# Performance work log

Hardware: AMD Instinct MI355X
Metric: run time of the kernel (lower is better)

Reference implementation:

```python
import jax, jax.numpy as jnp
import numpy as np

EPS = 1e-5

def _proj(x, w, b, gamma, beta, mean, var):
    # 1x1 conv (einsum over channels) + BatchNorm (inference) ; Dropout is identity in eval.
    y = jnp.einsum('bchw,oc->bohw', x, w) + b[None, :, None, None]
    scale = gamma * jax.lax.rsqrt(var + EPS)
    shift = beta - mean * scale
    return y * scale[None, :, None, None] + shift[None, :, None, None]

def _make_layer(key, cin, cout):
    k1, k2, k3, k4 = jax.random.split(key, 4)
    w = jax.random.normal(k1, (cout, cin), jnp.float32) * (1.0 / np.sqrt(cin))
    b = jax.random.normal(k2, (cout,), jnp.float32) * 0.01
    gamma = 1.0 + 0.1 * jax.random.normal(k3, (cout,), jnp.float32)
    beta = 0.1 * jax.random.normal(k4, (cout,), jnp.float32)
    mean = 0.05 * jax.random.normal(jax.random.fold_in(k1, 7), (cout,), jnp.float32)
    var = 0.5 + jax.random.uniform(jax.random.fold_in(k2, 7), (cout,), jnp.float32)
    return w, b, gamma, beta, mean, var

def setup_inputs() -> dict:
    key = jax.random.key(0)
    B, C, Ci, H, W = 4, 128, 64, 64, 64
    ks = jax.random.split(key, 6)
    inp = {
        'x1': jax.random.normal(ks[0], (B, C, H, W), jnp.float32),
        'x2': jax.random.normal(ks[1], (B, C, H, W), jnp.float32),
    }
    for name, k, cin, cout in [('theta', ks[2], C, Ci), ('phi', ks[3], C, Ci),
                               ('g', ks[4], C, Ci), ('wout', ks[5], Ci, C)]:
        w, b, gm, bt, mn, vr = _make_layer(k, cin, cout)
        inp.update({f'{name}_w': w, f'{name}_b': b, f'{name}_g': gm,
                    f'{name}_beta': bt, f'{name}_m': mn, f'{name}_v': vr})
    return inp

def reference(x1, x2,
              theta_w, theta_b, theta_g, theta_beta, theta_m, theta_v,
              phi_w, phi_b, phi_g, phi_beta, phi_m, phi_v,
              g_w, g_b, g_g, g_beta, g_m, g_v,
              wout_w, wout_b, wout_g, wout_beta, wout_m, wout_v):
    B, C, H, W = x1.shape
    N = H * W
    theta_x1 = _proj(x1, theta_w, theta_b, theta_g, theta_beta, theta_m, theta_v).reshape(B, -1, N)  # [B,Ci,N]
    phi_x2 = _proj(x2, phi_w, phi_b, phi_g, phi_beta, phi_m, phi_v).reshape(B, -1, N)                # [B,Ci,N]
    g_x2 = _proj(x2, g_w, g_b, g_g, g_beta, g_m, g_v).reshape(B, -1, N)                              # [B,Ci,N]
    # attention_map[b, n, m] = sum_c theta[b,c,n] * phi[b,c,m]
    attn = jax.nn.softmax(jnp.einsum('bcn,bcm->bnm', theta_x1, phi_x2), axis=-1)  # [B,N,N]
    out = jnp.einsum('bnm,bcm->bcn', attn, g_x2).reshape(B, -1, H, W)             # [B,Ci,H,W]
    out = _proj(out, wout_w, wout_b, wout_g, wout_beta, wout_m, wout_v)           # [B,C,H,W]
    return jnp.concatenate((out, x1), axis=1)                                     # [B,2C,H,W]
```

## Files before the change

### kernel.cpp

```cpp
#include <hip/hip_runtime.h>
#include <stdint.h>
#include <stddef.h>

#define EPS   1e-5f
#define CINCH 128
#define CI    64
#define NPIX  4096
#define KSPL  8
#define LOG2E 1.44269504088896340736f

typedef __bf16 bf16_t;
typedef _Float16 f16_t;
typedef bf16_t bf16x8 __attribute__((ext_vector_type(8)));
typedef f16_t  f16x8  __attribute__((ext_vector_type(8)));
typedef float  f32x4  __attribute__((ext_vector_type(4)));

typedef __attribute__((address_space(3))) unsigned int lds_u32;
typedef __attribute__((address_space(1))) const unsigned int glb_u32;

__device__ __forceinline__ f32x4 mfma16(bf16x8 a, bf16x8 b, f32x4 c) {
  return __builtin_amdgcn_mfma_f32_16x16x32_bf16(a, b, c, 0, 0, 0);
}
__device__ __forceinline__ f32x4 fzero4() {
  f32x4 z = {0.f, 0.f, 0.f, 0.f};
  return z;
}
__device__ __forceinline__ void gload16(const void* g, void* l) {
  __builtin_amdgcn_global_load_lds((glb_u32*)g, (lds_u32*)l, 16, 0, 0);
}


__global__ __launch_bounds__(256) void proj_theta(
    const float* __restrict__ x1,
    const float* __restrict__ w,  const float* __restrict__ bb,
    const float* __restrict__ gm, const float* __restrict__ bt,
    const float* __restrict__ mn, const float* __restrict__ vr,
    bf16_t* __restrict__ thetaT_h, bf16_t* __restrict__ thetaT_l,
    float* __restrict__ out)
{
  __shared__ float wT[CINCH][CI];
  __shared__ float bfold[CI];
  __shared__ __align__(16) char ubuf[CINCH * 32 * 4];
  float (*xs)[32]    = (float(*)[32])ubuf;
  float (*tileF)[68] = (float(*)[68])ubuf;

  const int tid = threadIdx.x;
  const int b   = blockIdx.y;
  const int n0  = blockIdx.x * 32;

  for (int idx = tid; idx < CI * CINCH; idx += 256) {
    const int o = idx & 63, c = idx >> 6;
    const float sc = gm[o] * rsqrtf(vr[o] + EPS);
    wT[c][o] = w[o * CINCH + c] * sc * LOG2E;
    if (c == 0) bfold[o] = (bb[o] * sc + bt[o] - mn[o] * sc) * LOG2E;
  }

  {
    const float* xsrc = x1 + (size_t)b * CINCH * NPIX + n0;
    float* osrc = out + ((size_t)b * 256 + 128) * NPIX + n0;
#pragma unroll
    for (int i = 0; i < 4; ++i) {
      const int idx = i * 256 + tid;
      const int c = idx >> 3, p = idx & 7;
      const f32x4 v = *(const f32x4*)(xsrc + (size_t)c * NPIX + p * 4);
      *(f32x4*)&xs[c][p * 4] = v;
      *(f32x4*)(osrc + (size_t)c * NPIX + p * 4) = v;
    }
  }
  __syncthreads();

  const int px = tid & 31;
  const int og = tid >> 5;
  float acc[8];
#pragma unroll
  for (int j = 0; j < 8; ++j) acc[j] = 0.f;

#pragma unroll 4
  for (int c0 = 0; c0 < CINCH; c0 += 4) {
    float xv[4];
#pragma unroll
    for (int cc = 0; cc < 4; ++cc) xv[cc] = xs[c0 + cc][px];
#pragma unroll
    for (int cc = 0; cc < 4; ++cc) {
      const f32x4 w0 = *(const f32x4*)&wT[c0 + cc][og * 8];
      const f32x4 w1 = *(const f32x4*)&wT[c0 + cc][og * 8 + 4];
#pragma unroll
      for (int j = 0; j < 4; ++j) {
        acc[j]     += w0[j] * xv[cc];
        acc[j + 4] += w1[j] * xv[cc];
      }
    }
  }
  __syncthreads();
#pragma unroll
  for (int j = 0; j < 8; ++j) tileF[px][og * 8 + j] = acc[j] + bfold[og * 8 + j];
  __syncthreads();

  {
    const int px2 = tid >> 3, ogs = tid & 7;
    bf16x8 hv, lv;
#pragma unroll
    for (int j = 0; j < 8; ++j) {
      const float v = tileF[px2][ogs * 8 + j];
      const bf16_t h = (bf16_t)v;
      hv[j] = h;
      lv[j] = (bf16_t)(v - (float)h);
    }
    const size_t base = ((size_t)b * NPIX + n0 + px2) * CI + ogs * 8;
    *(bf16x8*)(thetaT_h + base) = hv;
    *(bf16x8*)(thetaT_l + base) = lv;
  }
}

__global__ __launch_bounds__(256) void proj_phi(
    const float* __restrict__ x2,
    const float* __restrict__ w,  const float* __restrict__ bb,
    const float* __restrict__ gm, const float* __restrict__ bt,
    const float* __restrict__ mn, const float* __restrict__ vr,
    bf16_t* __restrict__ phiT_h, bf16_t* __restrict__ phiT_l)
{
  __shared__ float wT[CINCH][CI];
  __shared__ float bfold[CI];
  __shared__ __align__(16) char ubuf[CINCH * 32 * 4];
  float (*xs)[32]    = (float(*)[32])ubuf;
  float (*tileF)[68] = (float(*)[68])ubuf;

  const int tid = threadIdx.x;
  const int b   = blockIdx.y;
  const int n0  = blockIdx.x * 32;

  for (int idx = tid; idx < CI * CINCH; idx += 256) {
    const int o = idx & 63, c = idx >> 6;
    const float sc = gm[o] * rsqrtf(vr[o] + EPS);
    wT[c][o] = w[o * CINCH + c] * sc;
    if (c == 0) bfold[o] = bb[o] * sc + bt[o] - mn[o] * sc;
  }
  {
    const float* xsrc = x2 + (size_t)b * CINCH * NPIX + n0;
#pragma unroll
    for (int i = 0; i < 4; ++i) {
      const int idx = i * 256 + tid;
      const int c = idx >> 3, p = idx & 7;
      *(f32x4*)&xs[c][p * 4] = *(const f32x4*)(xsrc + (size_t)c * NPIX + p * 4);
    }
  }
  __syncthreads();

  const int px = tid & 31;
  const int og = tid >> 5;
  float acc[8];
#pragma unroll
  for (int j = 0; j < 8; ++j) acc[j] = 0.f;

#pragma unroll 4
  for (int c0 = 0; c0 < CINCH; c0 += 4) {
    float xv[4];
#pragma unroll
    for (int cc = 0; cc < 4; ++cc) xv[cc] = xs[c0 + cc][px];
#pragma unroll
    for (int cc = 0; cc < 4; ++cc) {
      const f32x4 w0 = *(const f32x4*)&wT[c0 + cc][og * 8];
      const f32x4 w1 = *(const f32x4*)&wT[c0 + cc][og * 8 + 4];
#pragma unroll
      for (int j = 0; j < 4; ++j) {
        acc[j]     += w0[j] * xv[cc];
        acc[j + 4] += w1[j] * xv[cc];
      }
    }
  }
  __syncthreads();
#pragma unroll
  for (int j = 0; j < 8; ++j) tileF[px][og * 8 + j] = acc[j] + bfold[og * 8 + j];
  __syncthreads();

  {
    const int px2 = tid >> 3, ogs = tid & 7;
    const int n = n0 + px2;
    bf16x8 hv, lv;
#pragma unroll
    for (int j = 0; j < 8; ++j) {
      const float v = tileF[px2][ogs * 8 + j];
      const bf16_t h = (bf16_t)v;
      hv[j] = h;
      lv[j] = (bf16_t)(v - (float)h);
    }
    const size_t rowb = ((size_t)b * NPIX + n) * 128;
    const int byte = (ogs * 16) ^ ((n & 7) << 4);
    *(bf16x8*)((char*)phiT_h + rowb + byte) = hv;
    *(bf16x8*)((char*)phiT_l + rowb + byte) = lv;
  }
}

__global__ __launch_bounds__(256) void proj_g(
    const float* __restrict__ x2,
    const float* __restrict__ w,  const float* __restrict__ bb,
    const float* __restrict__ gm, const float* __restrict__ bt,
    const float* __restrict__ mn, const float* __restrict__ vr,
    bf16_t* __restrict__ g_cm)
{
  __shared__ float wT[CINCH][CI];
  __shared__ float bfold[CI];
  __shared__ __align__(16) char ubuf[CINCH * 32 * 4];
  float (*xs)[32] = (float(*)[32])ubuf;
  float (*gT)[33] = (float(*)[33])ubuf;

  const int tid = threadIdx.x;
  const int b   = blockIdx.y;
  const int n0  = blockIdx.x * 32;

  for (int idx = tid; idx < CI * CINCH; idx += 256) {
    const int o = idx & 63, c = idx >> 6;
    const float sc = gm[o] * rsqrtf(vr[o] + EPS);
    wT[c][o] = w[o * CINCH + c] * sc;
    if (c == 0) bfold[o] = bb[o] * sc + bt[o] - mn[o] * sc;
  }
  {
    const float* xsrc = x2 + (size_t)b * CINCH * NPIX + n0;
#pragma unroll
    for (int i = 0; i < 4; ++i) {
      const int idx = i * 256 + tid;
      const int c = idx >> 3, p = idx & 7;
      *(f32x4*)&xs[c][p * 4] = *(const f32x4*)(xsrc + (size_t)c * NPIX + p * 4);
    }
  }
  __syncthreads();

  const int px = tid & 31;
  const int og = tid >> 5;
  float acc[8];
#pragma unroll
  for (int j = 0; j < 8; ++j) acc[j] = 0.f;

#pragma unroll 4
  for (int c0 = 0; c0 < CINCH; c0 += 4) {
    float xv[4];
#pragma unroll
    for (int cc = 0; cc < 4; ++cc) xv[cc] = xs[c0 + cc][px];
#pragma unroll
    for (int cc = 0; cc < 4; ++cc) {
      const f32x4 w0 = *(const f32x4*)&wT[c0 + cc][og * 8];
      const f32x4 w1 = *(const f32x4*)&wT[c0 + cc][og * 8 + 4];
#pragma unroll
      for (int j = 0; j < 4; ++j) {
        acc[j]     += w0[j] * xv[cc];
        acc[j + 4] += w1[j] * xv[cc];
      }
    }
  }
  __syncthreads();
#pragma unroll
  for (int j = 0; j < 8; ++j) gT[og * 8 + j][px] = acc[j] + bfold[og * 8 + j];
  __syncthreads();

  {
    const int c = tid & 63, mgp = tid >> 6;
    bf16x8 gv;
#pragma unroll
    for (int j = 0; j < 8; ++j) gv[j] = (bf16_t)gT[c][mgp * 8 + j];
    *(bf16x8*)(g_cm + ((size_t)b * CI + c) * NPIX + n0 + mgp * 8) = gv;
  }
}

__global__ __launch_bounds__(512, 4) void flash_attn(
    const bf16_t* __restrict__ thetaT_h, const bf16_t* __restrict__ thetaT_l,
    const bf16_t* __restrict__ phiT_h,   const bf16_t* __restrict__ phiT_l,
    const bf16_t* __restrict__ g_cm,
    f16_t* __restrict__ Opart, float* __restrict__ mlbuf)
{
  __shared__ __attribute__((aligned(16))) char sK[2][16384];
  __shared__ __attribute__((aligned(16))) char sV[2][8192];
  __shared__ __attribute__((aligned(16))) char sP[8][4096];

  const int tid  = threadIdx.x;
  const int lane = tid & 63;
  const int wid  = tid >> 6;
  const int lrow = lane & 15;
  const int lhi  = lane >> 4;

  const int wg = blockIdx.x;
  const int b  = wg >> 7;
  const int rr = wg & 127;
  const int qt = rr >> 3;
  const int ks = rr & 7;
  const int q0 = qt * 256 + wid * 32;
  const int tg0 = ks * 8;

  const char* const srcPHb = (const char*)phiT_h + ((size_t)b * NPIX) * 128;
  const char* const srcPLb = (const char*)phiT_l + ((size_t)b * NPIX) * 128;
  const char* const srcVb  = (const char*)g_cm + (size_t)b * CI * NPIX * 2;

  const int vc = tid >> 3, vp = tid & 7;
  const size_t vsrcoff = (size_t)vc * (NPIX * 2) + ((vp * 16) ^ ((vc & 7) << 4));

  auto stage = [&](int buf, int tg) {
    const size_t rb = (size_t)tg * 8192;
    gload16(srcPHb + rb + tid * 16, sK[buf] + tid * 16);
    gload16(srcPLb + rb + tid * 16, sK[buf] + 8192 + tid * 16);
    gload16(srcVb + vsrcoff + (size_t)tg * 128, sV[buf] + tid * 16);
  };

  stage(0, tg0);

  bf16x8 qh[2][2], qlv[2][2];
  {
    const bf16_t* qbh = thetaT_h + ((size_t)b * NPIX + q0 + lrow) * CI + lhi * 8;
    const bf16_t* qbl = thetaT_l + ((size_t)b * NPIX + q0 + lrow) * CI + lhi * 8;
#pragma unroll
    for (int nt = 0; nt < 2; ++nt)
#pragma unroll
      for (int kk = 0; kk < 2; ++kk) {
        qh[nt][kk]  = *(const bf16x8*)(qbh + nt * 16 * CI + kk * 32);
        qlv[nt][kk] = *(const bf16x8*)(qbl + nt * 16 * CI + kk * 32);
      }
  }

  f32x4 oacc[2][4];
#pragma unroll
  for (int a = 0; a < 2; ++a)
#pragma unroll
    for (int c = 0; c < 4; ++c) oacc[a][c] = fzero4();

  float m_run[2] = {-1e30f, -1e30f};
  float l_run[2] = {0.f, 0.f};

  char* const Pw = sP[wid];

  __syncthreads();

  for (int t = 0; t < 8; ++t) {
    const int cur = t & 1;

    if (t) {
      asm volatile("s_waitcnt lgkmcnt(0)" ::: "memory");
      __builtin_amdgcn_s_barrier();
    }
    if (t < 7) {
      stage(cur ^ 1, tg0 + t + 1);
      asm volatile("s_waitcnt vmcnt(3)" ::: "memory");
    } else {
      asm volatile("s_waitcnt vmcnt(0)" ::: "memory");
    }
    __builtin_amdgcn_s_barrier();
    __builtin_amdgcn_sched_barrier(0);

    const char* const sKH = sK[cur];
    const char* const sKL = sK[cur] + 8192;
    const char* const sVc = sV[cur];

    f32x4 s[4][2];
#pragma unroll
    for (int mt = 0; mt < 4; ++mt)
#pragma unroll
      for (int nt = 0; nt < 2; ++nt) s[mt][nt] = fzero4();

    __builtin_amdgcn_s_setprio(1);
#pragma unroll
    for (int mt = 0; mt < 4; ++mt) {
      const int row = mt * 16 + lrow;
      const int swz = (row & 7) << 4;
#pragma unroll
      for (int kk = 0; kk < 2; ++kk) {
        const int byte = row * 128 + ((kk * 64 + lhi * 16) ^ swz);
        const bf16x8 aH = *(const bf16x8*)(sKH + byte);
        const bf16x8 aL = *(const bf16x8*)(sKL + byte);
#pragma unroll
        for (int nt = 0; nt < 2; ++nt) {
          s[mt][nt] = mfma16(aH, qh[nt][kk],  s[mt][nt]);
          s[mt][nt] = mfma16(aH, qlv[nt][kk], s[mt][nt]);
          s[mt][nt] = mfma16(aL, qh[nt][kk],  s[mt][nt]);
        }
      }
    }
    __builtin_amdgcn_s_setprio(0);

    float mx[2], a2[2];
#pragma unroll
    for (int nt = 0; nt < 2; ++nt) {
      float m1 = fmaxf(fmaxf(s[0][nt][0], s[0][nt][1]), fmaxf(s[0][nt][2], s[0][nt][3]));
      float m2 = fmaxf(fmaxf(s[1][nt][0], s[1][nt][1]), fmaxf(s[1][nt][2], s[1][nt][3]));
      float m3 = fmaxf(fmaxf(s[2][nt][0], s[2][nt][1]), fmaxf(s[2][nt][2], s[2][nt][3]));
      float m4 = fmaxf(fmaxf(s[3][nt][0], s[3][nt][1]), fmaxf(s[3][nt][2], s[3][nt][3]));
      float m = fmaxf(fmaxf(m1, m2), fmaxf(m3, m4));
      m = fmaxf(m, __shfl_xor(m, 16));
      m = fmaxf(m, __shfl_xor(m, 32));
      mx[nt] = m;
    }
    const bool up = !__all((mx[0] <= m_run[0] + 5.f) && (mx[1] <= m_run[1] + 5.f));
#pragma unroll
    for (int nt = 0; nt < 2; ++nt) {
      const float mnew  = up ? fmaxf(m_run[nt], mx[nt]) : m_run[nt];
      const float alpha = up ? exp2f(m_run[nt] - mnew) : 1.f;
      float lsum = 0.f;
#pragma unroll
      for (int mt = 0; mt < 4; ++mt)
#pragma unroll
        for (int r = 0; r < 4; ++r) {
          const float p = exp2f(s[mt][nt][r] - mnew);
          s[mt][nt][r] = p;
          lsum += p;
        }
      lsum += __shfl_xor(lsum, 16);
      lsum += __shfl_xor(lsum, 32);
      l_run[nt] = l_run[nt] * alpha + lsum;
      m_run[nt] = mnew;
      a2[nt] = alpha;
    }

    if (up) {
#pragma unroll
      for (int qt2 = 0; qt2 < 2; ++qt2) {
#pragma unroll
        for (int r = 0; r < 4; ++r) {
          const float av = __shfl(a2[qt2], lhi * 4 + r);
#pragma unroll
          for (int ct = 0; ct < 4; ++ct) oacc[qt2][ct][r] *= av;
        }
      }
    }

#pragma unroll
    for (int mt = 0; mt < 4; ++mt)
#pragma unroll
      for (int nt = 0; nt < 2; ++nt) {
        union { bf16_t h[4]; uint32_t u[2]; } pk;
#pragma unroll
        for (int r = 0; r < 4; ++r) pk.h[r] = (bf16_t)s[mt][nt][r];
        const int q    = nt * 16 + lrow;
        const int mloc = mt * 16 + lhi * 4;
        const int byte = q * 128 + ((mloc * 2) ^ ((q & 7) << 4));
        *(uint2*)(Pw + byte) = make_uint2(pk.u[0], pk.u[1]);
      }

    bf16x8 bV[2][4];
#pragma unroll
    for (int ct = 0; ct < 4; ++ct) {
      const int row = ct * 16 + lrow;
      const int swz = (row & 7) << 4;
#pragma unroll
      for (int kk = 0; kk < 2; ++kk)
        bV[kk][ct] = *(const bf16x8*)(sVc + row * 128 + ((kk * 64 + lhi * 16) ^ swz));
    }
    __builtin_amdgcn_s_setprio(1);
#pragma unroll
    for (int qt2 = 0; qt2 < 2; ++qt2) {
      const int q = qt2 * 16 + lrow;
#pragma unroll
      for (int kk = 0; kk < 2; ++kk) {
        const bf16x8 pfrag =
            *(const bf16x8*)(Pw + q * 128 + ((kk * 64 + lhi * 16) ^ ((q & 7) << 4)));
#pragma unroll
        for (int ct = 0; ct < 4; ++ct)
          oacc[qt2][ct] = mfma16(pfrag, bV[kk][ct], oacc[qt2][ct]);
      }
    }
    __builtin_amdgcn_s_setprio(0);
  }

  {
#pragma unroll
    for (int qt2 = 0; qt2 < 2; ++qt2)
#pragma unroll
      for (int ct = 0; ct < 4; ++ct)
#pragma unroll
        for (int r = 0; r < 4; ++r) {
          const int ql = qt2 * 16 + lhi * 4 + r;
          const int c  = ct * 16 + lrow;
          *(f16_t*)(Pw + (ql * 64 + c) * 2) = (f16_t)oacc[qt2][ct][r];
        }
    f16_t* const Ob = Opart + ((size_t)(b * KSPL + ks) * NPIX + q0) * 64;
#pragma unroll
    for (int i = 0; i < 4; ++i) {
      const int idx = i * 64 + lane;
      *(f16x8*)(Ob + idx * 8) = *(const f16x8*)(Pw + idx * 16);
    }
  }
  if (lhi < 2) {
    const int q = q0 + lhi * 16 + lrow;
    const size_t base = ((size_t)(b * KSPL + ks) * NPIX + q) * 2;
    mlbuf[base]     = m_run[lhi];
    mlbuf[base + 1] = l_run[lhi];
  }
}

__global__ __launch_bounds__(256) void merge_out(
    const f16_t* __restrict__ Opart, const float* __restrict__ mlbuf,
    const float* __restrict__ ww,  const float* __restrict__ wb,
    const float* __restrict__ wg,  const float* __restrict__ wbt,
    const float* __restrict__ wm,  const float* __restrict__ wvv,
    float* __restrict__ out)
{
  __shared__ float wlds[128][64];
  __shared__ float bfw[128];
  __shared__ float mrg[32][68];

  const int tid = threadIdx.x;
  const int b   = blockIdx.y;
  const int n0  = blockIdx.x * 32;

  for (int idx = tid; idx < 128 * 64; idx += 256) {
    const int o = idx >> 6, c = idx & 63;
    const float sc = wg[o] * rsqrtf(wvv[o] + EPS);
    wlds[o][c] = ww[o * 64 + c] * sc;
    if (c == 0) bfw[o] = wb[o] * sc + wbt[o] - wm[o] * sc;
  }

  {
    const int px = tid & 31;
    const int cg = tid >> 5;
    const int q  = n0 + px;
    float mk[KSPL], lk[KSPL];
#pragma unroll
    for (int ks = 0; ks < KSPL; ++ks) {
      const size_t base = ((size_t)(b * KSPL + ks) * NPIX + q) * 2;
      mk[ks] = mlbuf[base];
      lk[ks] = mlbuf[base + 1];
    }
    float M = mk[0];
#pragma unroll
    for (int ks = 1; ks < KSPL; ++ks) M = fmaxf(M, mk[ks]);
    float al[KSPL]; float den = 0.f;
#pragma unroll
    for (int ks = 0; ks < KSPL; ++ks) { al[ks] = exp2f(mk[ks] - M); den += al[ks] * lk[ks]; }
    const float inv = 1.f / den;
#pragma unroll
    for (int ks = 0; ks < KSPL; ++ks) al[ks] *= inv;

    float r[8];
#pragma unroll
    for (int j = 0; j < 8; ++j) r[j] = 0.f;
#pragma unroll
    for (int ks = 0; ks < KSPL; ++ks) {
      const f16x8 p = *(const f16x8*)(Opart +
          ((size_t)(b * KSPL + ks) * NPIX + q) * 64 + cg * 8);
#pragma unroll
      for (int j = 0; j < 8; ++j) r[j] += (float)p[j] * al[ks];
    }
#pragma unroll
    for (int j = 0; j < 8; ++j) mrg[px][cg * 8 + j] = r[j];
  }
  __syncthreads();

  const int px = tid & 31;
  const int oh = tid >> 5;
  float acc[16];
#pragma unroll
  for (int j = 0; j < 16; ++j) acc[j] = 0.f;

#pragma unroll 4
  for (int c0 = 0; c0 < 64; c0 += 4) {
    const f32x4 m4 = *(const f32x4*)&mrg[px][c0];
#pragma unroll
    for (int j = 0; j < 16; ++j) {
      const f32x4 w4 = *(const f32x4*)&wlds[oh * 16 + j][c0];
      acc[j] += w4[0] * m4[0] + w4[1] * m4[1] + w4[2] * m4[2] + w4[3] * m4[3];
    }
  }
#pragma unroll
  for (int j = 0; j < 16; ++j) {
    const int o = oh * 16 + j;
    out[((size_t)b * 256 + o) * NPIX + n0 + px] = acc[j] + bfw[o];
  }
}

extern "C" void kernel_launch(void* const* d_in, const int* in_sizes, int n_in,
                              void* d_out, int out_size, void* d_ws, size_t ws_size,
                              hipStream_t stream) {
  (void)in_sizes; (void)n_in; (void)out_size; (void)ws_size;
  const float* x1  = (const float*)d_in[0];
  const float* x2  = (const float*)d_in[1];
  const float* tw  = (const float*)d_in[2];
  const float* tb  = (const float*)d_in[3];
  const float* tg  = (const float*)d_in[4];
  const float* tbt = (const float*)d_in[5];
  const float* tm  = (const float*)d_in[6];
  const float* tv  = (const float*)d_in[7];
  const float* pw  = (const float*)d_in[8];
  const float* pb  = (const float*)d_in[9];
  const float* pg  = (const float*)d_in[10];
  const float* pbt = (const float*)d_in[11];
  const float* pm  = (const float*)d_in[12];
  const float* pv  = (const float*)d_in[13];
  const float* gw  = (const float*)d_in[14];
  const float* gb  = (const float*)d_in[15];
  const float* gg  = (const float*)d_in[16];
  const float* gbt = (const float*)d_in[17];
  const float* gmn = (const float*)d_in[18];
  const float* gv  = (const float*)d_in[19];
  const float* ww  = (const float*)d_in[20];
  const float* wb  = (const float*)d_in[21];
  const float* wg  = (const float*)d_in[22];
  const float* wbt = (const float*)d_in[23];
  const float* wm  = (const float*)d_in[24];
  const float* wv  = (const float*)d_in[25];

  float* out = (float*)d_out;
  char*  ws  = (char*)d_ws;
  bf16_t* thetaT_h = (bf16_t*)(ws);
  bf16_t* thetaT_l = (bf16_t*)(ws + (size_t)(2)  * 1048576);
  bf16_t* phiT_h   = (bf16_t*)(ws + (size_t)(4)  * 1048576);
  bf16_t* phiT_l   = (bf16_t*)(ws + (size_t)(6)  * 1048576);
  bf16_t* g_cm     = (bf16_t*)(ws + (size_t)(8)  * 1048576);
  f16_t*  Opart    = (f16_t*) (ws + (size_t)(10) * 1048576);
  float*  mlbuf    = (float*) (ws + (size_t)(26) * 1048576);

  dim3 gp(128, 4);
  proj_theta<<<gp, 256, 0, stream>>>(x1, tw, tb, tg, tbt, tm, tv,
                                     thetaT_h, thetaT_l, out);
  proj_phi<<<gp, 256, 0, stream>>>(x2, pw, pb, pg, pbt, pm, pv,
                                   phiT_h, phiT_l);
  proj_g<<<gp, 256, 0, stream>>>(x2, gw, gb, gg, gbt, gmn, gv, g_cm);
  flash_attn<<<512, 512, 0, stream>>>(thetaT_h, thetaT_l, phiT_h, phiT_l,
                                      g_cm, Opart, mlbuf);
  merge_out<<<gp, 256, 0, stream>>>(Opart, mlbuf, ww, wb, wg, wbt, wm, wv, out);
}
```

Baseline: 249.3 us.

## Fuse projection kernels and restructure flash attention to 256 threads, 4-way KV split

Merges the three theta/phi/g projection kernels into one kernel that stages x2 once and reuses it for both phi and g. The flash-attention kernel moves from 512-thread blocks with an 8-way key split to 256-thread blocks with a 4-way split and 16 KV tiles each. Its double-buffered staging is simplified to a syncthreads-based loop in place of the manual waitcnt/barrier pipeline. This cuts launch overhead, redundant loads and the partial-output merge traffic, but gives fewer waves per block and may lose load/compute overlap.

```diff
diff --git a/kernel.cpp b/kernel.cpp
--- a/kernel.cpp
+++ b/kernel.cpp
@@ -6,7 +6,7 @@
 #define CINCH 128
 #define CI    64
 #define NPIX  4096
-#define KSPL  8
+#define KSPL  4
 #define LOG2E 1.44269504088896340736f
 
 typedef __bf16 bf16_t;
@@ -30,78 +30,105 @@
 }
 
 
-__global__ __launch_bounds__(256) void proj_theta(
-    const float* __restrict__ x1,
-    const float* __restrict__ w,  const float* __restrict__ bb,
-    const float* __restrict__ gm, const float* __restrict__ bt,
-    const float* __restrict__ mn, const float* __restrict__ vr,
+__global__ __launch_bounds__(256) void proj_all(
+    const float* __restrict__ x1, const float* __restrict__ x2,
+    const float* __restrict__ tw, const float* __restrict__ tb,
+    const float* __restrict__ tg, const float* __restrict__ tbt,
+    const float* __restrict__ tm, const float* __restrict__ tv,
+    const float* __restrict__ pw, const float* __restrict__ pb,
+    const float* __restrict__ pg, const float* __restrict__ pbt,
+    const float* __restrict__ pm, const float* __restrict__ pv,
+    const float* __restrict__ gw, const float* __restrict__ gb,
+    const float* __restrict__ gg, const float* __restrict__ gbt,
+    const float* __restrict__ gmn, const float* __restrict__ gv,
     bf16_t* __restrict__ thetaT_h, bf16_t* __restrict__ thetaT_l,
-    float* __restrict__ out)
+    bf16_t* __restrict__ phiT_h,   bf16_t* __restrict__ phiT_l,
+    bf16_t* __restrict__ g_cm,     float* __restrict__ out)
 {
   __shared__ float wT[CINCH][CI];
-  __shared__ float bfold[CI];
-  __shared__ __align__(16) char ubuf[CINCH * 32 * 4];
-  float (*xs)[32]    = (float(*)[32])ubuf;
-  float (*tileF)[68] = (float(*)[68])ubuf;
+  __shared__ float bf[CI];
+  __shared__ float xs[CINCH][32];
+  __shared__ __align__(16) char tbuf[32 * 68 * 4];
+  float (*tF)[68] = (float(*)[68])tbuf;
+  float (*gT)[33] = (float(*)[33])tbuf;
 
   const int tid = threadIdx.x;
   const int b   = blockIdx.y;
   const int n0  = blockIdx.x * 32;
-
-  for (int idx = tid; idx < CI * CINCH; idx += 256) {
-    const int o = idx & 63, c = idx >> 6;
-    const float sc = gm[o] * rsqrtf(vr[o] + EPS);
-    wT[c][o] = w[o * CINCH + c] * sc * LOG2E;
-    if (c == 0) bfold[o] = (bb[o] * sc + bt[o] - mn[o] * sc) * LOG2E;
-  }
-
+  const int px  = tid & 31;
+  const int og  = tid >> 5;
+
+  auto loadW = [&](const float* w, const float* bb_, const float* gm_,
+                   const float* bt_, const float* mn_, const float* vr_,
+                   float mul) {
+    for (int idx = tid; idx < CI * CINCH; idx += 256) {
+      const int o = idx & 63, c = idx >> 6;
+      const float sc = gm_[o] * rsqrtf(vr_[o] + EPS);
+      wT[c][o] = w[o * CINCH + c] * sc * mul;
+      if (c == 0) bf[o] = (bb_[o] * sc + bt_[o] - mn_[o] * sc) * mul;
+    }
+  };
+  auto stageX = [&](const float* x) {
+    const float* xsrc = x + (size_t)b * CINCH * NPIX + n0;
+#pragma unroll
+    for (int i = 0; i < 4; ++i) {
+      const int idx = i * 256 + tid;
+      const int c = idx >> 3, p = idx & 7;
+      *(f32x4*)&xs[c][p * 4] = *(const f32x4*)(xsrc + (size_t)c * NPIX + p * 4);
+    }
+  };
+  auto compute = [&](float* acc) {
+#pragma unroll
+    for (int j = 0; j < 8; ++j) acc[j] = 0.f;
+#pragma unroll 4
+    for (int c0 = 0; c0 < CINCH; c0 += 4) {
+      float xv[4];
+#pragma unroll
+      for (int cc = 0; cc < 4; ++cc) xv[cc] = xs[c0 + cc][px];
+#pragma unroll
+      for (int cc = 0; cc < 4; ++cc) {
+        const f32x4 w0 = *(const f32x4*)&wT[c0 + cc][og * 8];
+        const f32x4 w1 = *(const f32x4*)&wT[c0 + cc][og * 8 + 4];
+#pragma unroll
+        for (int j = 0; j < 4; ++j) {
+          acc[j]     += w0[j] * xv[cc];
+          acc[j + 4] += w1[j] * xv[cc];
+        }
+      }
+    }
+#pragma unroll
+    for (int j = 0; j < 8; ++j) acc[j] += bf[og * 8 + j];
+  };
+
+  float acc[8];
+
+  loadW(tw, tb, tg, tbt, tm, tv, LOG2E);
   {
     const float* xsrc = x1 + (size_t)b * CINCH * NPIX + n0;
-    float* osrc = out + ((size_t)b * 256 + 128) * NPIX + n0;
+    float* odst = out + ((size_t)b * 256 + 128) * NPIX + n0;
 #pragma unroll
     for (int i = 0; i < 4; ++i) {
       const int idx = i * 256 + tid;
       const int c = idx >> 3, p = idx & 7;
       const f32x4 v = *(const f32x4*)(xsrc + (size_t)c * NPIX + p * 4);
       *(f32x4*)&xs[c][p * 4] = v;
-      *(f32x4*)(osrc + (size_t)c * NPIX + p * 4) = v;
-    }
-  }
-  __syncthreads();
-
-  const int px = tid & 31;
-  const int og = tid >> 5;
-  float acc[8];
-#pragma unroll
-  for (int j = 0; j < 8; ++j) acc[j] = 0.f;
-
-#pragma unroll 4
-  for (int c0 = 0; c0 < CINCH; c0 += 4) {
-    float xv[4];
-#pragma unroll
-    for (int cc = 0; cc < 4; ++cc) xv[cc] = xs[c0 + cc][px];
-#pragma unroll
-    for (int cc = 0; cc < 4; ++cc) {
-      const f32x4 w0 = *(const f32x4*)&wT[c0 + cc][og * 8];
-      const f32x4 w1 = *(const f32x4*)&wT[c0 + cc][og * 8 + 4];
-#pragma unroll
-      for (int j = 0; j < 4; ++j) {
-        acc[j]     += w0[j] * xv[cc];
-        acc[j + 4] += w1[j] * xv[cc];
-      }
-    }
-  }
-  __syncthreads();
-#pragma unroll
-  for (int j = 0; j < 8; ++j) tileF[px][og * 8 + j] = acc[j] + bfold[og * 8 + j];
-  __syncthreads();
-
+      *(f32x4*)(odst + (size_t)c * NPIX + p * 4) = v;
+    }
+  }
+  __syncthreads();
+  compute(acc);
+  __syncthreads();
+#pragma unroll
+  for (int j = 0; j < 8; ++j) tF[px][og * 8 + j] = acc[j];
+  loadW(pw, pb, pg, pbt, pm, pv, 1.f);
+  stageX(x2);
+  __syncthreads();
   {
     const int px2 = tid >> 3, ogs = tid & 7;
     bf16x8 hv, lv;
 #pragma unroll
     for (int j = 0; j < 8; ++j) {
-      const float v = tileF[px2][ogs * 8 + j];
+      const float v = tF[px2][ogs * 8 + j];
       const bf16_t h = (bf16_t)v;
       hv[j] = h;
       lv[j] = (bf16_t)(v - (float)h);
@@ -110,76 +137,20 @@
     *(bf16x8*)(thetaT_h + base) = hv;
     *(bf16x8*)(thetaT_l + base) = lv;
   }
-}
-
-__global__ __launch_bounds__(256) void proj_phi(
-    const float* __restrict__ x2,
-    const float* __restrict__ w,  const float* __restrict__ bb,
-    const float* __restrict__ gm, const float* __restrict__ bt,
-    const float* __restrict__ mn, const float* __restrict__ vr,
-    bf16_t* __restrict__ phiT_h, bf16_t* __restrict__ phiT_l)
-{
-  __shared__ float wT[CINCH][CI];
-  __shared__ float bfold[CI];
-  __shared__ __align__(16) char ubuf[CINCH * 32 * 4];
-  float (*xs)[32]    = (float(*)[32])ubuf;
-  float (*tileF)[68] = (float(*)[68])ubuf;
-
-  const int tid = threadIdx.x;
-  const int b   = blockIdx.y;
-  const int n0  = blockIdx.x * 32;
-
-  for (int idx = tid; idx < CI * CINCH; idx += 256) {
-    const int o = idx & 63, c = idx >> 6;
-    const float sc = gm[o] * rsqrtf(vr[o] + EPS);
-    wT[c][o] = w[o * CINCH + c] * sc;
-    if (c == 0) bfold[o] = bb[o] * sc + bt[o] - mn[o] * sc;
-  }
-  {
-    const float* xsrc = x2 + (size_t)b * CINCH * NPIX + n0;
-#pragma unroll
-    for (int i = 0; i < 4; ++i) {
-      const int idx = i * 256 + tid;
-      const int c = idx >> 3, p = idx & 7;
-      *(f32x4*)&xs[c][p * 4] = *(const f32x4*)(xsrc + (size_t)c * NPIX + p * 4);
-    }
-  }
-  __syncthreads();
-
-  const int px = tid & 31;
-  const int og = tid >> 5;
-  float acc[8];
-#pragma unroll
-  for (int j = 0; j < 8; ++j) acc[j] = 0.f;
-
-#pragma unroll 4
-  for (int c0 = 0; c0 < CINCH; c0 += 4) {
-    float xv[4];
-#pragma unroll
-    for (int cc = 0; cc < 4; ++cc) xv[cc] = xs[c0 + cc][px];
-#pragma unroll
-    for (int cc = 0; cc < 4; ++cc) {
-      const f32x4 w0 = *(const f32x4*)&wT[c0 + cc][og * 8];
-      const f32x4 w1 = *(const f32x4*)&wT[c0 + cc][og * 8 + 4];
-#pragma unroll
-      for (int j = 0; j < 4; ++j) {
-        acc[j]     += w0[j] * xv[cc];
-        acc[j + 4] += w1[j] * xv[cc];
-      }
-    }
-  }
-  __syncthreads();
-#pragma unroll
-  for (int j = 0; j < 8; ++j) tileF[px][og * 8 + j] = acc[j] + bfold[og * 8 + j];
-  __syncthreads();
-
+
+  compute(acc);
+  __syncthreads();
+#pragma unroll
+  for (int j = 0; j < 8; ++j) tF[px][og * 8 + j] = acc[j];
+  loadW(gw, gb, gg, gbt, gmn, gv, 1.f);
+  __syncthreads();
   {
     const int px2 = tid >> 3, ogs = tid & 7;
     const int n = n0 + px2;
     bf16x8 hv, lv;
 #pragma unroll
     for (int j = 0; j < 8; ++j) {
-      const float v = tileF[px2][ogs * 8 + j];
+      const float v = tF[px2][ogs * 8 + j];
       const bf16_t h = (bf16_t)v;
       hv[j] = h;
       lv[j] = (bf16_t)(v - (float)h);
@@ -189,69 +160,12 @@
     *(bf16x8*)((char*)phiT_h + rowb + byte) = hv;
     *(bf16x8*)((char*)phiT_l + rowb + byte) = lv;
   }
-}
-
-__global__ __launch_bounds__(256) void proj_g(
-    const float* __restrict__ x2,
-    const float* __restrict__ w,  const float* __restrict__ bb,
-    const float* __restrict__ gm, const float* __restrict__ bt,
-    const float* __restrict__ mn, const float* __restrict__ vr,
-    bf16_t* __restrict__ g_cm)
-{
-  __shared__ float wT[CINCH][CI];
-  __shared__ float bfold[CI];
-  __shared__ __align__(16) char ubuf[CINCH * 32 * 4];
-  float (*xs)[32] = (float(*)[32])ubuf;
-  float (*gT)[33] = (float(*)[33])ubuf;
-
-  const int tid = threadIdx.x;
-  const int b   = blockIdx.y;
-  const int n0  = blockIdx.x * 32;
-
-  for (int idx = tid; idx < CI * CINCH; idx += 256) {
-    const int o = idx & 63, c = idx >> 6;
-    const float sc = gm[o] * rsqrtf(vr[o] + EPS);
-    wT[c][o] = w[o * CINCH + c] * sc;
-    if (c == 0) bfold[o] = bb[o] * sc + bt[o] - mn[o] * sc;
-  }
-  {
-    const float* xsrc = x2 + (size_t)b * CINCH * NPIX + n0;
-#pragma unroll
-    for (int i = 0; i < 4; ++i) {
-      const int idx = i * 256 + tid;
-      const int c = idx >> 3, p = idx & 7;
-      *(f32x4*)&xs[c][p * 4] = *(const f32x4*)(xsrc + (size_t)c * NPIX + p * 4);
-    }
-  }
-  __syncthreads();
-
-  const int px = tid & 31;
-  const int og = tid >> 5;
-  float acc[8];
-#pragma unroll
-  for (int j = 0; j < 8; ++j) acc[j] = 0.f;
-
-#pragma unroll 4
-  for (int c0 = 0; c0 < CINCH; c0 += 4) {
-    float xv[4];
-#pragma unroll
-    for (int cc = 0; cc < 4; ++cc) xv[cc] = xs[c0 + cc][px];
-#pragma unroll
-    for (int cc = 0; cc < 4; ++cc) {
-      const f32x4 w0 = *(const f32x4*)&wT[c0 + cc][og * 8];
-      const f32x4 w1 = *(const f32x4*)&wT[c0 + cc][og * 8 + 4];
-#pragma unroll
-      for (int j = 0; j < 4; ++j) {
-        acc[j]     += w0[j] * xv[cc];
-        acc[j + 4] += w1[j] * xv[cc];
-      }
-    }
-  }
-  __syncthreads();
-#pragma unroll
-  for (int j = 0; j < 8; ++j) gT[og * 8 + j][px] = acc[j] + bfold[og * 8 + j];
-  __syncthreads();
-
+
+  compute(acc);
+  __syncthreads();
+#pragma unroll
+  for (int j = 0; j < 8; ++j) gT[og * 8 + j][px] = acc[j];
+  __syncthreads();
   {
     const int c = tid & 63, mgp = tid >> 6;
     bf16x8 gv;
@@ -261,15 +175,14 @@
   }
 }
 
-__global__ __launch_bounds__(512, 4) void flash_attn(
+__global__ __launch_bounds__(256, 2) void flash_attn(
     const bf16_t* __restrict__ thetaT_h, const bf16_t* __restrict__ thetaT_l,
     const bf16_t* __restrict__ phiT_h,   const bf16_t* __restrict__ phiT_l,
     const bf16_t* __restrict__ g_cm,
     f16_t* __restrict__ Opart, float* __restrict__ mlbuf)
 {
-  __shared__ __attribute__((aligned(16))) char sK[2][16384];
-  __shared__ __attribute__((aligned(16))) char sV[2][8192];
-  __shared__ __attribute__((aligned(16))) char sP[8][4096];
+  __shared__ __attribute__((aligned(16))) char sT[2][24576];
+  __shared__ __attribute__((aligned(16))) char sP[4][4096];
 
   const int tid  = threadIdx.x;
   const int lane = tid & 63;
@@ -280,26 +193,33 @@
   const int wg = blockIdx.x;
   const int b  = wg >> 7;
   const int rr = wg & 127;
-  const int qt = rr >> 3;
-  const int ks = rr & 7;
-  const int q0 = qt * 256 + wid * 32;
-  const int tg0 = ks * 8;
+  const int qt = rr >> 2;
+  const int ks = rr & 3;
+  const int q0 = qt * 128 + wid * 32;
+  const int t0 = ks * 16;
 
   const char* const srcPHb = (const char*)phiT_h + ((size_t)b * NPIX) * 128;
   const char* const srcPLb = (const char*)phiT_l + ((size_t)b * NPIX) * 128;
   const char* const srcVb  = (const char*)g_cm + (size_t)b * CI * NPIX * 2;
 
-  const int vc = tid >> 3, vp = tid & 7;
-  const size_t vsrcoff = (size_t)vc * (NPIX * 2) + ((vp * 16) ^ ((vc & 7) << 4));
-
-  auto stage = [&](int buf, int tg) {
-    const size_t rb = (size_t)tg * 8192;
-    gload16(srcPHb + rb + tid * 16, sK[buf] + tid * 16);
-    gload16(srcPLb + rb + tid * 16, sK[buf] + 8192 + tid * 16);
-    gload16(srcVb + vsrcoff + (size_t)tg * 128, sV[buf] + tid * 16);
+  auto stage = [&](int buf, int tile) {
+    const size_t rb = (size_t)tile * 8192;
+    char* const dst = sT[buf];
+    gload16(srcPHb + rb + tid * 16,         dst + tid * 16);
+    gload16(srcPHb + rb + (256 + tid) * 16, dst + (256 + tid) * 16);
+    gload16(srcPLb + rb + tid * 16,         dst + 8192 + tid * 16);
+    gload16(srcPLb + rb + (256 + tid) * 16, dst + 8192 + (256 + tid) * 16);
+#pragma unroll
+    for (int k = 0; k < 2; ++k) {
+      const int c2 = k * 256 + tid;
+      const int row = c2 >> 3, part = c2 & 7;
+      gload16(srcVb + (size_t)row * (NPIX * 2) + tile * 128 +
+                  ((part * 16) ^ ((row & 7) << 4)),
+              dst + 16384 + c2 * 16);
+    }
   };
 
-  stage(0, tg0);
+  stage(0, t0);
 
   bf16x8 qh[2][2], qlv[2][2];
   {
@@ -327,25 +247,13 @@
 
   __syncthreads();
 
-  for (int t = 0; t < 8; ++t) {
-    const int cur = t & 1;
-
-    if (t) {
-      asm volatile("s_waitcnt lgkmcnt(0)" ::: "memory");
-      __builtin_amdgcn_s_barrier();
-    }
-    if (t < 7) {
-      stage(cur ^ 1, tg0 + t + 1);
-      asm volatile("s_waitcnt vmcnt(3)" ::: "memory");
-    } else {
-      asm volatile("s_waitcnt vmcnt(0)" ::: "memory");
-    }
-    __builtin_amdgcn_s_barrier();
-    __builtin_amdgcn_sched_barrier(0);
-
-    const char* const sKH = sK[cur];
-    const char* const sKL = sK[cur] + 8192;
-    const char* const sVc = sV[cur];
+  for (int tt = 0; tt < 16; ++tt) {
+    const int cur = tt & 1;
+    if (tt < 15) stage(cur ^ 1, t0 + tt + 1);
+
+    const char* const sKH = sT[cur];
+    const char* const sKL = sT[cur] + 8192;
+    const char* const sVc = sT[cur] + 16384;
 
     f32x4 s[4][2];
 #pragma unroll
@@ -454,6 +362,8 @@
       }
     }
     __builtin_amdgcn_s_setprio(0);
+
+    if (tt < 15) __syncthreads();
   }
 
   {
@@ -601,15 +511,16 @@
   bf16_t* phiT_l   = (bf16_t*)(ws + (size_t)(6)  * 1048576);
   bf16_t* g_cm     = (bf16_t*)(ws + (size_t)(8)  * 1048576);
   f16_t*  Opart    = (f16_t*) (ws + (size_t)(10) * 1048576);
-  float*  mlbuf    = (float*) (ws + (size_t)(26) * 1048576);
+  float*  mlbuf    = (float*) (ws + (size_t)(18) * 1048576);
 
   dim3 gp(128, 4);
-  proj_theta<<<gp, 256, 0, stream>>>(x1, tw, tb, tg, tbt, tm, tv,
-                                     thetaT_h, thetaT_l, out);
-  proj_phi<<<gp, 256, 0, stream>>>(x2, pw, pb, pg, pbt, pm, pv,
-                                   phiT_h, phiT_l);
-  proj_g<<<gp, 256, 0, stream>>>(x2, gw, gb, gg, gbt, gmn, gv, g_cm);
-  flash_attn<<<512, 512, 0, stream>>>(thetaT_h, thetaT_l, phiT_h, phiT_l,
+  proj_all<<<gp, 256, 0, stream>>>(x1, x2,
+                                   tw, tb, tg, tbt, tm, tv,
+                                   pw, pb, pg, pbt, pm, pv,
+                                   gw, gb, gg, gbt, gmn, gv,
+                                   thetaT_h, thetaT_l, phiT_h, phiT_l,
+                                   g_cm, out);
+  flash_attn<<<512, 256, 0, stream>>>(thetaT_h, thetaT_l, phiT_h, phiT_l,
                                       g_cm, Opart, mlbuf);
   merge_out<<<gp, 256, 0, stream>>>(Opart, mlbuf, ww, wb, wg, wbt, wm, wv, out);
 }
```

Measured after the change: 226.6 us. -9.1%, faster.
